# Kernel optimization log

Hardware: AMD Instinct MI355X
Metric: run time of the kernel (lower is better)

The kernel has to match this reference:

```python
import jax, jax.numpy as jnp
import numpy as np
import math

B, KLEN, QLEN, KDIM, QDIM, ADIM, H = 16, 2048, 512, 512, 512, 512, 4
D_K = ADIM // H
SCALE = math.sqrt(ADIM)
INIT_R = -4.0


def setup_inputs() -> dict:
    key = jax.random.key(0)
    k0, k1, k2, k3, k4 = jax.random.split(key, 5)
    # Xavier-ish scaled init for projection weights (stored as [in, out] for x @ W)
    wk = jax.random.normal(k3, (KDIM, ADIM), dtype=jnp.float32) * (1.0 / math.sqrt(KDIM))
    wq = jax.random.normal(k4, (QDIM, ADIM), dtype=jnp.float32) * (1.0 / math.sqrt(QDIM))
    return {
        "key_in": jax.random.normal(k0, (B, KLEN, KDIM), dtype=jnp.float32),
        "query": jax.random.normal(k1, (B, QLEN, QDIM), dtype=jnp.float32),
        "mask": jax.random.randint(k2, (B, QLEN, KLEN), 0, 2, dtype=jnp.int32),
        "Wk": wk,
        "bk": jnp.zeros((ADIM,), dtype=jnp.float32),
        "Wq": wq,
        "bq": jnp.zeros((ADIM,), dtype=jnp.float32),
        "r": jnp.array([INIT_R], dtype=jnp.float32),
    }


def reference(key_in, query, mask, Wk, bk, Wq, bq, r):
    bs, klen, _ = key_in.shape
    qlen = query.shape[1]
    # key/query projections -> [B, len, H, d_k]
    k = (key_in @ Wk + bk).reshape(bs, klen, H, D_K)
    q = (query @ Wq + bq).reshape(bs, qlen, H, D_K)
    # scaled dot-product energy [B, qlen, klen, H] + scalar offset r
    e = jnp.einsum('bihd,bjhd->bijh', q, k) / SCALE + r[0]
    neg_inf = jnp.finfo(e.dtype).min
    e = jnp.where(mask[..., None] == 0, neg_inf, e)
    # permute to [B, H, qlen, klen]
    return jnp.transpose(e, (0, 3, 1, 2))
```

## Files before the change

### kernel.cpp

```cpp
#include <hip/hip_runtime.h>
#include <stdint.h>

typedef unsigned short u16;
typedef __attribute__((ext_vector_type(8))) short bf16x8;
typedef __attribute__((ext_vector_type(4))) float f32x4;
typedef __attribute__((ext_vector_type(4))) unsigned short u16x4;
typedef __attribute__((ext_vector_type(4))) int i32x4;

#define INV_SCALE 0.04419417382415922f
#define MASKED_F32 (-3.0e38f)

__device__ __forceinline__ u16 f2bf(float f) {
  uint32_t u = __float_as_uint(f);
  u += 0x7fffu + ((u >> 16) & 1u);
  return (u16)(u >> 16);
}

__global__ void prep_kernel(const float* __restrict__ ina, u16* __restrict__ outa,
                            const float* __restrict__ inb, u16* __restrict__ outb,
                            int n4a,
                            const float* __restrict__ Wk, u16* __restrict__ WTk,
                            const float* __restrict__ Wq, u16* __restrict__ WTq) {
  __shared__ float tile[32][33];
  if (blockIdx.x < 20480) {
    int idx = blockIdx.x * 256 + threadIdx.x;
    const float* in = ina;
    u16* out = outa;
    if (idx >= n4a) { idx -= n4a; in = inb; out = outb; }
    f32x4 v = __builtin_nontemporal_load(reinterpret_cast<const f32x4*>(in) + idx);
    u16x4 h;
#pragma unroll
    for (int j = 0; j < 4; ++j) h[j] = f2bf(v[j]);
    reinterpret_cast<u16x4*>(out)[idx] = h;
    return;
  }
  const int bid2 = blockIdx.x - 20480;
  const int bx = bid2 & 15, by = (bid2 >> 4) & 15, z = bid2 >> 8;
  const float* W = z ? Wq : Wk;
  u16* WT = z ? WTq : WTk;
  const int tx = threadIdx.x & 31, ty = threadIdx.x >> 5;
#pragma unroll
  for (int r = 0; r < 32; r += 8)
    tile[ty + r][tx] = W[(by * 32 + ty + r) * 512 + bx * 32 + tx];
  __syncthreads();
#pragma unroll
  for (int r = 0; r < 32; r += 8) {
    const int n = bx * 32 + ty + r, k = by * 32 + tx;
    WT[n * 512 + k] = f2bf(tile[tx][ty + r]);
  }
}

__device__ __forceinline__ void stage_tile(const u16* g_base, u16* l_base) {
  const int t = threadIdx.x;
#pragma unroll
  for (int i = 0; i < 2; ++i) {
    const int s = t + i * 256;
    const int row = s >> 2;
    const int gc = (s & 3) ^ ((row >> 1) & 3);
    const u16* g = g_base + row * 512 + gc * 8;
    __builtin_amdgcn_global_load_lds(
        (__attribute__((address_space(1))) void*)(u16*)g,
        (__attribute__((address_space(3))) void*)(l_base + s * 8),
        16, 0, 0);
  }
}

template <int KTILES>
__device__ __forceinline__ void gemm_core(const u16* A, const u16* B,
                                          u16* lds, f32x4 acc[4][4],
                                          int wm, int wn, int l16, int q) {
  stage_tile(A, lds);
  stage_tile(B, lds + 4096);
  __syncthreads();
#pragma unroll
  for (int kt = 0; kt < KTILES; ++kt) {
    u16* lA = lds + (kt & 1) * 8192;
    u16* lB = lA + 4096;
    if (kt + 1 < KTILES) {
      u16* nxt = lds + ((kt + 1) & 1) * 8192;
      stage_tile(A + (kt + 1) * 32, nxt);
      stage_tile(B + (kt + 1) * 32, nxt + 4096);
    }
    bf16x8 af[4], bfr[4];
#pragma unroll
    for (int mt = 0; mt < 4; ++mt) {
      const int row = wm + mt * 16 + l16;
      const int s = (row << 2) + (q ^ ((row >> 1) & 3));
      af[mt] = *reinterpret_cast<const bf16x8*>(lA + s * 8);
    }
#pragma unroll
    for (int nt = 0; nt < 4; ++nt) {
      const int row = wn + nt * 16 + l16;
      const int s = (row << 2) + (q ^ ((row >> 1) & 3));
      bfr[nt] = *reinterpret_cast<const bf16x8*>(lB + s * 8);
    }
#pragma unroll
    for (int mt = 0; mt < 4; ++mt)
#pragma unroll
      for (int nt = 0; nt < 4; ++nt)
        acc[mt][nt] = __builtin_amdgcn_mfma_f32_16x16x32_bf16(af[mt], bfr[nt], acc[mt][nt], 0, 0, 0);
    __syncthreads();
  }
}

__global__ __launch_bounds__(256)
void proj_kernel(const u16* __restrict__ Xk, const u16* __restrict__ WTk,
                 const float* __restrict__ bk, u16* __restrict__ Ok,
                 const u16* __restrict__ Xq, const u16* __restrict__ WTq,
                 const float* __restrict__ bq, u16* __restrict__ Oq) {
  __shared__ u16 lds[4 * 4096];
  int bid = (blockIdx.x & 7) * 160 + (blockIdx.x >> 3);
  const u16 *X = Xk, *WT = WTk; const float* bias = bk; u16* O = Ok;
  if (bid >= 1024) { bid -= 1024; X = Xq; WT = WTq; bias = bq; O = Oq; }
  const int m0 = (bid >> 2) * 128;
  const int n0 = (bid & 3) * 128;
  const int lane = threadIdx.x & 63;
  const int wave = threadIdx.x >> 6;
  const int wm = (wave >> 1) * 64, wn = (wave & 1) * 64;
  const int l16 = lane & 15, q = lane >> 4;

  f32x4 acc[4][4];
#pragma unroll
  for (int a = 0; a < 4; ++a)
#pragma unroll
    for (int b = 0; b < 4; ++b) acc[a][b] = (f32x4){0.f, 0.f, 0.f, 0.f};

  gemm_core<16>(WT + (size_t)n0 * 512, X + (size_t)m0 * 512,
                lds, acc, wm, wn, l16, q);

#pragma unroll
  for (int nt = 0; nt < 4; ++nt) {
    const size_t gm = (size_t)(m0 + wn + nt * 16 + l16);
#pragma unroll
    for (int mt = 0; mt < 4; ++mt) {
      const int gn0 = n0 + wm + mt * 16 + q * 4;
      const f32x4 bv = *reinterpret_cast<const f32x4*>(bias + gn0);
      u16x4 o;
#pragma unroll
      for (int rg = 0; rg < 4; ++rg) o[rg] = f2bf(acc[mt][nt][rg] + bv[rg]);
      *reinterpret_cast<u16x4*>(O + gm * 512 + gn0) = o;
    }
  }
}

__global__ __launch_bounds__(256)
void energy_kernel(const u16* __restrict__ Q, const u16* __restrict__ K,
                   const int* __restrict__ mask, const float* __restrict__ r,
                   float* __restrict__ out) {
  __shared__ u16 lds[4 * 4096];
  int bid = (blockIdx.x & 7) * 512 + (blockIdx.x >> 3);
  const int it = bid & 3;  bid >>= 2;
  const int h = bid & 3;   bid >>= 2;
  const int jt = bid & 15; bid >>= 4;
  const int b = bid;
  const int lane = threadIdx.x & 63;
  const int wave = threadIdx.x >> 6;
  const int wm = (wave >> 1) * 64, wn = (wave & 1) * 64;
  const int l16 = lane & 15, q = lane >> 4;

  f32x4 acc[4][4];
#pragma unroll
  for (int a = 0; a < 4; ++a)
#pragma unroll
    for (int c = 0; c < 4; ++c) acc[a][c] = (f32x4){0.f, 0.f, 0.f, 0.f};

  const size_t qoff = (size_t)(b * 512 + it * 128) * 512 + h * 128;
  const size_t koff = (size_t)(b * 2048 + jt * 128) * 512 + h * 128;
  gemm_core<4>(K + koff, Q + qoff, lds, acc, wm, wn, l16, q);

  const float rv = r[0];
  const size_t obase = ((size_t)(b * 4 + h)) * 512 * 2048;
  const size_t mbase = ((size_t)b) * 512 * 2048;
#pragma unroll
  for (int nt = 0; nt < 4; ++nt) {
    const int i = it * 128 + wn + nt * 16 + l16;
    const size_t rowo = obase + (size_t)i * 2048;
    const size_t rowm = mbase + (size_t)i * 2048;
#pragma unroll
    for (int mt = 0; mt < 4; ++mt) {
      const int j0 = jt * 128 + wm + mt * 16 + q * 4;
      const i32x4 mv = *reinterpret_cast<const i32x4*>(mask + rowm + j0);
      const f32x4 a = acc[mt][nt];
      f32x4 o;
#pragma unroll
      for (int rg = 0; rg < 4; ++rg) {
        float e = a[rg] * INV_SCALE + rv;
        e = fminf(fmaxf(e, -1e30f), 1e30f);
        o[rg] = (mv[rg] == 0) ? MASKED_F32 : e;
      }
      *reinterpret_cast<f32x4*>(out + rowo + j0) = o;
    }
  }
}

extern "C" void kernel_launch(void* const* d_in, const int* in_sizes, int n_in,
                              void* d_out, int out_size, void* d_ws, size_t ws_size,
                              hipStream_t stream) {
  const float* key_in = (const float*)d_in[0];
  const float* query  = (const float*)d_in[1];
  const int*   mask   = (const int*)d_in[2];
  const float* Wk     = (const float*)d_in[3];
  const float* bk     = (const float*)d_in[4];
  const float* Wq     = (const float*)d_in[5];
  const float* bq     = (const float*)d_in[6];
  const float* r      = (const float*)d_in[7];

  u16* xkhi = (u16*)d_out;
  u16* xqhi = xkhi + 16777216;
  u16* wkT  = xqhi + 4194304;
  u16* wqT  = wkT + 262144;

  u16* khi = (u16*)d_in[0];
  u16* qhi = (u16*)d_in[1];

  prep_kernel<<<20992, 256, 0, stream>>>(key_in, xkhi, query, xqhi, 4194304,
                                         Wk, wkT, Wq, wqT);
  proj_kernel<<<1280, 256, 0, stream>>>(xkhi, wkT, bk, khi, xqhi, wqT, bq, qhi);
  energy_kernel<<<4096, 256, 0, stream>>>(qhi, khi, mask, r, (float*)d_out);
}
```

Baseline: 481.2 us.

## Make energy kernel persistent over key tiles with register-resident Q fragments

The energy kernel now launches 512 blocks instead of 4096. Each block loads its 128-row Q tile once into registers and then loops over 8 key tiles (half the key length), double-buffering the full 128x128 K tile in LDS while it computes and writes the masked output for the previous tile. This removes redundant Q reloads and per-block launch and prologue overhead. In exchange it uses more registers (64 extra VGPRs for the Q fragments) and twice the LDS, which lowers occupancy, and 512 blocks may underfill the GPU for a store-bound kernel. The MFMA inner step is also factored into a helper for the projection GEMM.

```diff
diff --git a/kernel.cpp b/kernel.cpp
--- a/kernel.cpp
+++ b/kernel.cpp
@@ -65,6 +65,29 @@
   }
 }
 
+__device__ __forceinline__ void mfma_step(const u16* lA, const u16* lB,
+                                          f32x4 acc[4][4],
+                                          int wm, int wn, int l16, int q) {
+  bf16x8 af[4], bfr[4];
+#pragma unroll
+  for (int mt = 0; mt < 4; ++mt) {
+    const int row = wm + mt * 16 + l16;
+    const int s = (row << 2) + (q ^ ((row >> 1) & 3));
+    af[mt] = *reinterpret_cast<const bf16x8*>(lA + s * 8);
+  }
+#pragma unroll
+  for (int nt = 0; nt < 4; ++nt) {
+    const int row = wn + nt * 16 + l16;
+    const int s = (row << 2) + (q ^ ((row >> 1) & 3));
+    bfr[nt] = *reinterpret_cast<const bf16x8*>(lB + s * 8);
+  }
+#pragma unroll
+  for (int mt = 0; mt < 4; ++mt)
+#pragma unroll
+    for (int nt = 0; nt < 4; ++nt)
+      acc[mt][nt] = __builtin_amdgcn_mfma_f32_16x16x32_bf16(af[mt], bfr[nt], acc[mt][nt], 0, 0, 0);
+}
+
 template <int KTILES>
 __device__ __forceinline__ void gemm_core(const u16* A, const u16* B,
                                           u16* lds, f32x4 acc[4][4],
@@ -81,24 +104,7 @@
       stage_tile(A + (kt + 1) * 32, nxt);
       stage_tile(B + (kt + 1) * 32, nxt + 4096);
     }
-    bf16x8 af[4], bfr[4];
-#pragma unroll
-    for (int mt = 0; mt < 4; ++mt) {
-      const int row = wm + mt * 16 + l16;
-      const int s = (row << 2) + (q ^ ((row >> 1) & 3));
-      af[mt] = *reinterpret_cast<const bf16x8*>(lA + s * 8);
-    }
-#pragma unroll
-    for (int nt = 0; nt < 4; ++nt) {
-      const int row = wn + nt * 16 + l16;
-      const int s = (row << 2) + (q ^ ((row >> 1) & 3));
-      bfr[nt] = *reinterpret_cast<const bf16x8*>(lB + s * 8);
-    }
-#pragma unroll
-    for (int mt = 0; mt < 4; ++mt)
-#pragma unroll
-      for (int nt = 0; nt < 4; ++nt)
-        acc[mt][nt] = __builtin_amdgcn_mfma_f32_16x16x32_bf16(af[mt], bfr[nt], acc[mt][nt], 0, 0, 0);
+    mfma_step(lA, lB, acc, wm, wn, l16, q);
     __syncthreads();
   }
 }
@@ -147,49 +153,98 @@
 void energy_kernel(const u16* __restrict__ Q, const u16* __restrict__ K,
                    const int* __restrict__ mask, const float* __restrict__ r,
                    float* __restrict__ out) {
-  __shared__ u16 lds[4 * 4096];
-  int bid = (blockIdx.x & 7) * 512 + (blockIdx.x >> 3);
+  __shared__ u16 lds[2 * 16384];
+  int bid = (blockIdx.x & 7) * 64 + (blockIdx.x >> 3);
   const int it = bid & 3;  bid >>= 2;
-  const int h = bid & 3;   bid >>= 2;
-  const int jt = bid & 15; bid >>= 4;
-  const int b = bid;
+  const int h  = bid & 3;  bid >>= 2;
+  const int jh = bid & 1;  bid >>= 1;
+  const int b  = bid;
   const int lane = threadIdx.x & 63;
   const int wave = threadIdx.x >> 6;
   const int wm = (wave >> 1) * 64, wn = (wave & 1) * 64;
   const int l16 = lane & 15, q = lane >> 4;
 
-  f32x4 acc[4][4];
-#pragma unroll
-  for (int a = 0; a < 4; ++a)
-#pragma unroll
-    for (int c = 0; c < 4; ++c) acc[a][c] = (f32x4){0.f, 0.f, 0.f, 0.f};
-
-  const size_t qoff = (size_t)(b * 512 + it * 128) * 512 + h * 128;
-  const size_t koff = (size_t)(b * 2048 + jt * 128) * 512 + h * 128;
-  gemm_core<4>(K + koff, Q + qoff, lds, acc, wm, wn, l16, q);
+  const u16* Qp = Q + (size_t)(b * 512 + it * 128) * 512 + h * 128;
+#pragma unroll
+  for (int kt = 0; kt < 4; ++kt)
+    stage_tile(Qp + kt * 32, lds + kt * 4096);
+  __syncthreads();
+  bf16x8 qf[4][4];
+#pragma unroll
+  for (int kt = 0; kt < 4; ++kt)
+#pragma unroll
+    for (int nt = 0; nt < 4; ++nt) {
+      const int row = wn + nt * 16 + l16;
+      const int s = (row << 2) + (q ^ ((row >> 1) & 3));
+      qf[kt][nt] = *reinterpret_cast<const bf16x8*>(lds + kt * 4096 + s * 8);
+    }
+  __syncthreads();
+
+  const u16* Kp = K + (size_t)(b * 2048 + jh * 1024) * 512 + h * 128;
+#pragma unroll
+  for (int kt = 0; kt < 4; ++kt)
+    stage_tile(Kp + kt * 32, lds + kt * 4096);
+  __syncthreads();
 
   const float rv = r[0];
   const size_t obase = ((size_t)(b * 4 + h)) * 512 * 2048;
   const size_t mbase = ((size_t)b) * 512 * 2048;
-#pragma unroll
-  for (int nt = 0; nt < 4; ++nt) {
-    const int i = it * 128 + wn + nt * 16 + l16;
-    const size_t rowo = obase + (size_t)i * 2048;
-    const size_t rowm = mbase + (size_t)i * 2048;
-#pragma unroll
-    for (int mt = 0; mt < 4; ++mt) {
-      const int j0 = jt * 128 + wm + mt * 16 + q * 4;
-      const i32x4 mv = *reinterpret_cast<const i32x4*>(mask + rowm + j0);
-      const f32x4 a = acc[mt][nt];
-      f32x4 o;
-#pragma unroll
-      for (int rg = 0; rg < 4; ++rg) {
-        float e = a[rg] * INV_SCALE + rv;
-        e = fminf(fmaxf(e, -1e30f), 1e30f);
-        o[rg] = (mv[rg] == 0) ? MASKED_F32 : e;
+
+  for (int jt = 0; jt < 8; ++jt) {
+    u16* cur = lds + (jt & 1) * 16384;
+    u16* nxt = lds + ((jt + 1) & 1) * 16384;
+    if (jt + 1 < 8) {
+#pragma unroll
+      for (int kt = 0; kt < 4; ++kt)
+        stage_tile(Kp + (size_t)(jt + 1) * 128 * 512 + kt * 32, nxt + kt * 4096);
+    }
+
+    f32x4 acc[4][4];
+#pragma unroll
+    for (int a = 0; a < 4; ++a)
+#pragma unroll
+      for (int c = 0; c < 4; ++c) acc[a][c] = (f32x4){0.f, 0.f, 0.f, 0.f};
+
+#pragma unroll
+    for (int kt = 0; kt < 4; ++kt) {
+      const u16* lA = cur + kt * 4096;
+      bf16x8 af[4];
+#pragma unroll
+      for (int mt = 0; mt < 4; ++mt) {
+        const int row = wm + mt * 16 + l16;
+        const int s = (row << 2) + (q ^ ((row >> 1) & 3));
+        af[mt] = *reinterpret_cast<const bf16x8*>(lA + s * 8);
       }
-      *reinterpret_cast<f32x4*>(out + rowo + j0) = o;
-    }
+#pragma unroll
+      for (int mt = 0; mt < 4; ++mt)
+#pragma unroll
+        for (int nt = 0; nt < 4; ++nt)
+          acc[mt][nt] = __builtin_amdgcn_mfma_f32_16x16x32_bf16(
+              af[mt], qf[kt][nt], acc[mt][nt], 0, 0, 0);
+    }
+
+    const int jbase = jh * 1024 + jt * 128;
+#pragma unroll
+    for (int nt = 0; nt < 4; ++nt) {
+      const int i = it * 128 + wn + nt * 16 + l16;
+      const size_t rowo = obase + (size_t)i * 2048;
+      const size_t rowm = mbase + (size_t)i * 2048;
+#pragma unroll
+      for (int mt = 0; mt < 4; ++mt) {
+        const int j0 = jbase + wm + mt * 16 + q * 4;
+        const i32x4 mv = *reinterpret_cast<const i32x4*>(mask + rowm + j0);
+        const f32x4 a = acc[mt][nt];
+        f32x4 o;
+#pragma unroll
+        for (int rg = 0; rg < 4; ++rg) {
+          float e = a[rg] * INV_SCALE + rv;
+          e = fminf(fmaxf(e, -1e30f), 1e30f);
+          o[rg] = (mv[rg] == 0) ? MASKED_F32 : e;
+        }
+        *reinterpret_cast<f32x4*>(out + rowo + j0) = o;
+      }
+    }
+    __syncthreads();
   }
 }
 
@@ -216,5 +271,5 @@
   prep_kernel<<<20992, 256, 0, stream>>>(key_in, xkhi, query, xqhi, 4194304,
                                          Wk, wkT, Wq, wqT);
   proj_kernel<<<1280, 256, 0, stream>>>(xkhi, wkT, bk, khi, xqhi, wqT, bq, qhi);
-  energy_kernel<<<4096, 256, 0, stream>>>(qhi, khi, mask, r, (float*)d_out);
-}
+  energy_kernel<<<512, 256, 0, stream>>>(qhi, khi, mask, r, (float*)d_out);
+}
```

Measured after the change: 506.3 us. +5.2%, slower.
